# Optimization experiments

Hardware: AMD Instinct MI355X
Metric: run time of the kernel (lower is better)

The kernel has to match this reference:

```python
import jax, jax.numpy as jnp
import numpy as np

B, S, E, HD = 32, 1024, 768, 64
NUM_IMAGE_PATCHES = 49


def setup_inputs() -> dict:
    key = jax.random.key(0)
    ks = jax.random.split(key, 9)
    w = 0.02
    return {
        "decoder_sequence": jax.random.normal(ks[0], (B, S, E), dtype=jnp.float32),
        "Wq": jax.random.normal(ks[1], (E, HD), dtype=jnp.float32) * w,
        "bq": jnp.zeros((HD,), dtype=jnp.float32),
        "Wk": jax.random.normal(ks[2], (E, HD), dtype=jnp.float32) * w,
        "bk": jnp.zeros((HD,), dtype=jnp.float32),
        "Wv": jax.random.normal(ks[3], (E, HD), dtype=jnp.float32) * w,
        "bv": jnp.zeros((HD,), dtype=jnp.float32),
        "input_sequence_length": 975,
        "padding_mask": jax.random.randint(ks[4], (B, 1, S), 0, 2).astype(bool),
    }


def reference(decoder_sequence, Wq, bq, Wk, bk, Wv, bv, input_sequence_length, padding_mask):
    # single-head projections: [B,S,E] @ [E,HD] -> [B,S,HD]
    Q = decoder_sequence @ Wq + bq
    K = decoder_sequence @ Wk + bk
    V = decoder_sequence @ Wv + bv

    scores = jnp.einsum('bid,bjd->bij', Q, K) / jnp.sqrt(jnp.float32(HD))

    # mask: image-patch rows (i < 49) fully unmasked; text region is causal
    # (mask[49:,49:] = triu(-inf, diag=1)), i.e. -inf where i >= 49 and j > i.
    i = jnp.arange(S)[:, None]
    j = jnp.arange(S)[None, :]
    causal_bad = (i >= NUM_IMAGE_PATCHES) & (j > i)  # [S,S]
    scores = jnp.where(causal_bad[None, :, :], -jnp.inf, scores)

    # padding mask on keys, broadcast over queries: [B,1,S] -> [B,S,S]
    scores = jnp.where(padding_mask, -jnp.inf, scores)

    A = jax.nn.softmax(scores, axis=-1)
    H = jnp.einsum('bij,bjd->bid', A, V)
    return H
```

## Files before the change

kernel.cpp:

```cpp
#include <hip/hip_runtime.h>
#include <stdint.h>
#include <stddef.h>


typedef __attribute__((ext_vector_type(8))) short bf16x8;
typedef __attribute__((ext_vector_type(4))) float f32x4;

#define NIP 49
#define QSCALE 0.18033688011112042f

#define GLDS16(g, l)                                      \
  __builtin_amdgcn_global_load_lds(                       \
      (const __attribute__((address_space(1))) void*)(g), \
      (__attribute__((address_space(3))) void*)(l), 16, 0, 0)

__device__ __forceinline__ short f2b(float f) {
  union { float f; uint32_t u; } c; c.f = f;
  uint32_t u = c.u;
  uint32_t r = (u + 0x7fffu + ((u >> 16) & 1u)) >> 16;
  return (short)(uint16_t)r;
}

__device__ __forceinline__ uint32_t pk2(float lo, float hi) {
  uint32_t r;
  asm("v_cvt_pk_bf16_f32 %0, %1, %2" : "=v"(r) : "v"(lo), "v"(hi));
  return r;
}

__global__ __launch_bounds__(256) void wt_kernel(
    const float* __restrict__ Wq, const float* __restrict__ Wk,
    const float* __restrict__ Wv, const int* __restrict__ pad,
    short* __restrict__ Wt, float* __restrict__ padneg) {
  int idx = blockIdx.x * 256 + threadIdx.x;
  int m = idx / 49152;
  int idx2 = idx - m * 49152;
  int k = idx2 >> 6, n = idx2 & 63;
  const float* W = (m == 0) ? Wq : (m == 1) ? Wk : Wv;
  Wt[(size_t)(m * 64 + n) * 768 + k] = f2b(W[idx2]);
  if (idx < 32768) padneg[idx] = pad[idx] ? -16384.f : 0.f;
}

__global__ __launch_bounds__(256) void proj_kernel(
    const float* __restrict__ X, const float* __restrict__ bq,
    const float* __restrict__ bk, const float* __restrict__ bv,
    const short* __restrict__ Wt, short* __restrict__ Qg,
    short* __restrict__ Kg, short* __restrict__ Vt) {
  const int tid = threadIdx.x;
  const int wid = tid >> 6, lane = tid & 63;
  const int l15 = lane & 15, q4 = lane >> 4;
  const int r0 = blockIdx.x * 64;

  const float* xrow = X + (size_t)(r0 + wid * 16 + l15) * 768;
  float4 xa[2][4];
  auto xload = [&](int slot, int st) {
    const int kb = st * 64 + q4 * 8;
#pragma unroll
    for (int h = 0; h < 2; ++h) {
      xa[slot][h * 2 + 0] = *(const float4*)(xrow + kb + h * 32);
      xa[slot][h * 2 + 1] = *(const float4*)(xrow + kb + h * 32 + 4);
    }
  };
  auto mkfrag = [&](int slot, int h) {
    union { uint32_t u[4]; bf16x8 v; } r;
    const float4 a = xa[slot][h * 2], b = xa[slot][h * 2 + 1];
    r.u[0] = pk2(a.x, a.y); r.u[1] = pk2(a.z, a.w);
    r.u[2] = pk2(b.x, b.y); r.u[3] = pk2(b.z, b.w);
    return r.v;
  };

  const short* wrow = Wt + (size_t)l15 * 768 + q4 * 8;

  f32x4 acc[12];
#pragma unroll
  for (int c = 0; c < 12; ++c) acc[c] = (f32x4){0.f, 0.f, 0.f, 0.f};

  xload(0, 0);
  xload(1, 1);

#pragma unroll
  for (int st = 0; st < 12; ++st) {
    const int cur = st & 1;
    const bf16x8 a0 = mkfrag(cur, 0);
    const bf16x8 a1 = mkfrag(cur, 1);
    if (st + 2 < 12) xload(cur, st + 2);
#pragma unroll
    for (int c = 0; c < 12; ++c) {
      const short* wp = wrow + (size_t)c * 12288 + st * 64;
      const bf16x8 b0 = *(const bf16x8*)(wp);
      const bf16x8 b1 = *(const bf16x8*)(wp + 32);
      acc[c] = __builtin_amdgcn_mfma_f32_16x16x32_bf16(a0, b0, acc[c], 0, 0, 0);
      acc[c] = __builtin_amdgcn_mfma_f32_16x16x32_bf16(a1, b1, acc[c], 0, 0, 0);
    }
  }

  const int b = r0 >> 10, s0 = r0 & 1023;
#pragma unroll
  for (int c = 0; c < 12; ++c) {
    const int mtx = c >> 2;
    const int h = (c & 3) * 16 + l15;
    if (mtx < 2) {
      const float bias = (mtx == 0 ? bq : bk)[h];
      short* op = (mtx == 0) ? Qg : Kg;
#pragma unroll
      for (int rr = 0; rr < 4; ++rr) {
        int row = r0 + wid * 16 + q4 * 4 + rr;
        float v = acc[c][rr] + bias;
        if (mtx == 0) v *= QSCALE;
        op[(size_t)row * 64 + h] = f2b(v);
      }
    } else {
      const float bias = bv[h];
      uint2 sv;
      sv.x = pk2(acc[c][0] + bias, acc[c][1] + bias);
      sv.y = pk2(acc[c][2] + bias, acc[c][3] + bias);
      *(uint2*)(Vt + ((size_t)(b * 64 + h) << 10) + s0 + wid * 16 + q4 * 4) = sv;
    }
  }
}

__global__ __launch_bounds__(256, 2) void attn_kernel(
    const short* __restrict__ Qg, const short* __restrict__ Kg,
    const short* __restrict__ Vt, const float* __restrict__ padneg,
    float* __restrict__ out) {
  __shared__ short lK[2][2][128][32];
  __shared__ short lV[2][4][64][32];
  __shared__ short lOnes[16][32];

  const int b = blockIdx.x;
  const int level = blockIdx.y;
  const int t = (level == 0) ? 0 : 16 - level;
  const int tid = threadIdx.x;
  const int wid = tid >> 6, lane = tid & 63;
  const int l15 = lane & 15, q4 = lane >> 4;
  const int qs = t * 64;
  const size_t base = (size_t)b * 1024;
  const int nkt = (t == 0) ? 8 : (t / 2 + 1);

  {
    int i0 = tid, i1 = tid + 256;
    ((short*)lOnes)[i0] = ((i0 >> 5) == 0) ? (short)0x3F80 : (short)0;
    if (i1 < 512) ((short*)lOnes)[i1] = ((i1 >> 5) == 0) ? (short)0x3F80 : (short)0;
  }

  const short* qrow = Qg + (base + qs + wid * 16 + l15) * 64;
  bf16x8 bq0 = *(const bf16x8*)(qrow + q4 * 8);
  bf16x8 bq1 = *(const bf16x8*)(qrow + 32 + q4 * 8);
  const int qi = qs + wid * 16 + l15;

  const int sr = lane >> 2, sc = (lane & 3) * 8;
  auto wlds_tile = [&](int buf, int kt) {
    const int kb = kt * 128;
#pragma unroll
    for (int i = 0; i < 4; ++i) {
      const int dh = i & 1, krow = wid * 32 + (i >> 1) * 16;
      GLDS16(Kg + (base + kb + krow + sr) * 64 + dh * 32 + sc,
             &lK[buf][dh][krow][0]);
    }
#pragma unroll
    for (int kq = 0; kq < 4; ++kq) {
      GLDS16(Vt + ((size_t)(b * 64 + wid * 16 + sr) << 10) + kb + kq * 32 + sc,
             &lV[buf][kq][wid * 16][0]);
    }
  };

  float4 pnv[8];
  auto pnload = [&](int kt) {
#pragma unroll
    for (int c = 0; c < 8; ++c)
      pnv[c] = *(const float4*)(padneg + base + kt * 128 + c * 16 + q4 * 4);
  };

  pnload(0);
  wlds_tile(0, 0);
  __syncthreads();

  f32x4 o[5];
#pragma unroll
  for (int c = 0; c < 5; ++c) o[c] = (f32x4){0.f, 0.f, 0.f, 0.f};

  for (int kt = 0; kt < nkt; ++kt) {
    const int cur = kt & 1;
    const int kb = kt * 128;

    f32x4 s4[8];
#pragma unroll
    for (int c = 0; c < 8; ++c)
      s4[c] = (f32x4){pnv[c].x, pnv[c].y, pnv[c].z, pnv[c].w};

    if (kt + 1 < nkt) {
      wlds_tile(cur ^ 1, kt + 1);
      pnload(kt + 1);
    }

#pragma unroll
    for (int c = 0; c < 8; ++c) {
      bf16x8 a0 = *(const bf16x8*)&lK[cur][0][c * 16 + l15][q4 * 8];
      s4[c] = __builtin_amdgcn_mfma_f32_16x16x32_bf16(a0, bq0, s4[c], 0, 0, 0);
      bf16x8 a1 = *(const bf16x8*)&lK[cur][1][c * 16 + l15][q4 * 8];
      s4[c] = __builtin_amdgcn_mfma_f32_16x16x32_bf16(a1, bq1, s4[c], 0, 0, 0);
    }

    const bool diag = (t == 0) ? (kt == 0) : (kt == nkt - 1);
    const bool img = (t == 0 && kt > 0);
#pragma unroll
    for (int c = 0; c < 8; ++c) {
#pragma unroll
      for (int rr = 0; rr < 4; ++rr) {
        float pv = exp2f(fminf(s4[c][rr], 80.f));
        if (diag) {
          int j = kb + c * 16 + q4 * 4 + rr;
          if (qi >= NIP && j > qi) pv = 0.f;
        }
        if (img) {
          if (qi >= NIP) pv = 0.f;
        }
        s4[c][rr] = pv;
      }
    }

#pragma unroll
    for (int m = 0; m < 4; ++m) {
      uint32_t w0 = pk2(s4[2 * m][0], s4[2 * m][1]);
      uint32_t w1 = pk2(s4[2 * m][2], s4[2 * m][3]);
      uint32_t w2 = pk2(s4[2 * m + 1][0], s4[2 * m + 1][1]);
      uint32_t w3 = pk2(s4[2 * m + 1][2], s4[2 * m + 1][3]);
      asm("v_permlane32_swap_b32 %0, %1" : "+v"(w0), "+v"(w2));
      asm("v_permlane32_swap_b32 %0, %1" : "+v"(w1), "+v"(w3));
      asm("v_permlane16_swap_b32 %0, %1" : "+v"(w0), "+v"(w2));
      asm("v_permlane16_swap_b32 %0, %1" : "+v"(w1), "+v"(w3));
      union { uint32_t u[4]; bf16x8 v; } af;
      af.u[0] = w0; af.u[1] = w1; af.u[2] = w2; af.u[3] = w3;
#pragma unroll
      for (int c = 0; c < 5; ++c) {
        bf16x8 bv = (c < 4) ? *(const bf16x8*)&lV[cur][m][c * 16 + l15][q4 * 8]
                            : *(const bf16x8*)&lOnes[l15][q4 * 8];
        o[c] = __builtin_amdgcn_mfma_f32_16x16x32_bf16(af.v, bv, o[c], 0, 0, 0);
      }
    }
    __syncthreads();
  }

#pragma unroll
  for (int rr = 0; rr < 4; ++rr) {
    float l = __shfl(o[4][rr], lane & 48, 64);
    const float inv = (l > 0.f) ? 1.0f / l : 0.f;
    const size_t row = base + qs + wid * 16 + q4 * 4 + rr;
#pragma unroll
    for (int c = 0; c < 4; ++c)
      out[row * 64 + c * 16 + l15] = o[c][rr] * inv;
  }
}

extern "C" void kernel_launch(void* const* d_in, const int* in_sizes, int n_in,
                              void* d_out, int out_size, void* d_ws, size_t ws_size,
                              hipStream_t stream) {
  const float* X  = (const float*)d_in[0];
  const float* Wq = (const float*)d_in[1];
  const float* bq = (const float*)d_in[2];
  const float* Wk = (const float*)d_in[3];
  const float* bk = (const float*)d_in[4];
  const float* Wv = (const float*)d_in[5];
  const float* bv = (const float*)d_in[6];
  const int* pad  = (const int*)d_in[8];
  float* out = (float*)d_out;

  short* Qg = (short*)d_ws;
  short* Kg = Qg + 32768 * 64;
  short* Vt = Kg + 32768 * 64;
  short* Wt = Vt + 32768 * 64;
  float* padneg = (float*)(Wt + 147456);

  wt_kernel<<<576, 256, 0, stream>>>(Wq, Wk, Wv, pad, Wt, padneg);
  proj_kernel<<<512, 256, 0, stream>>>(X, bq, bk, bv, Wt, Qg, Kg, Vt);
  attn_kernel<<<dim3(32, 16), 256, 0, stream>>>(Qg, Kg, Vt, padneg, out);
}
```

Baseline: 243.5 us.

## Double per-wave row tile in projection and register-prefetch weight fragments

The projection kernel now has each wave compute two 16-row tiles instead of one, so every loaded weight fragment feeds two MFMAs. Weight fragments are prefetched into a double-buffered register array one k-step ahead, alongside the X loads. The grid is halved to 256 blocks with launch_bounds(256,1). The aim is to cut redundant global/L2 weight traffic and hide load latency, at the cost of much higher register pressure (48 accumulators plus 48 weight vectors) and fewer waves in flight.

```diff
diff --git a/kernel.cpp b/kernel.cpp
--- a/kernel.cpp
+++ b/kernel.cpp
@@ -31,16 +31,16 @@
     const float* __restrict__ Wq, const float* __restrict__ Wk,
     const float* __restrict__ Wv, const int* __restrict__ pad,
     short* __restrict__ Wt, float* __restrict__ padneg) {
-  int idx = blockIdx.x * 256 + threadIdx.x;
-  int m = idx / 49152;
-  int idx2 = idx - m * 49152;
+  int e = blockIdx.x * 256 + threadIdx.x;
+  int m = e / 49152;
+  int idx2 = e - m * 49152;
   int k = idx2 >> 6, n = idx2 & 63;
   const float* W = (m == 0) ? Wq : (m == 1) ? Wk : Wv;
   Wt[(size_t)(m * 64 + n) * 768 + k] = f2b(W[idx2]);
-  if (idx < 32768) padneg[idx] = pad[idx] ? -16384.f : 0.f;
-}
-
-__global__ __launch_bounds__(256) void proj_kernel(
+  if (e < 32768) padneg[e] = pad[e] ? -16384.f : 0.f;
+}
+
+__global__ __launch_bounds__(256, 1) void proj_kernel(
     const float* __restrict__ X, const float* __restrict__ bq,
     const float* __restrict__ bk, const float* __restrict__ bv,
     const short* __restrict__ Wt, short* __restrict__ Qg,
@@ -48,48 +48,68 @@
   const int tid = threadIdx.x;
   const int wid = tid >> 6, lane = tid & 63;
   const int l15 = lane & 15, q4 = lane >> 4;
-  const int r0 = blockIdx.x * 64;
-
-  const float* xrow = X + (size_t)(r0 + wid * 16 + l15) * 768;
-  float4 xa[2][4];
+  const int r0 = blockIdx.x * 128;
+  const int wr0 = r0 + wid * 32;
+
+  const float* xr0 = X + (size_t)(wr0 + l15) * 768;
+  const float* xr1 = xr0 + 16 * 768;
+  float4 xa[2][8];
   auto xload = [&](int slot, int st) {
     const int kb = st * 64 + q4 * 8;
 #pragma unroll
-    for (int h = 0; h < 2; ++h) {
-      xa[slot][h * 2 + 0] = *(const float4*)(xrow + kb + h * 32);
-      xa[slot][h * 2 + 1] = *(const float4*)(xrow + kb + h * 32 + 4);
-    }
-  };
-  auto mkfrag = [&](int slot, int h) {
+    for (int ks = 0; ks < 2; ++ks)
+#pragma unroll
+      for (int h = 0; h < 2; ++h) {
+        xa[slot][0 * 4 + ks * 2 + h] = *(const float4*)(xr0 + kb + ks * 32 + h * 4);
+        xa[slot][1 * 4 + ks * 2 + h] = *(const float4*)(xr1 + kb + ks * 32 + h * 4);
+      }
+  };
+  auto mkfrag = [&](int slot, int rt, int ks) {
     union { uint32_t u[4]; bf16x8 v; } r;
-    const float4 a = xa[slot][h * 2], b = xa[slot][h * 2 + 1];
+    const float4 a = xa[slot][rt * 4 + ks * 2 + 0];
+    const float4 b = xa[slot][rt * 4 + ks * 2 + 1];
     r.u[0] = pk2(a.x, a.y); r.u[1] = pk2(a.z, a.w);
     r.u[2] = pk2(b.x, b.y); r.u[3] = pk2(b.z, b.w);
     return r.v;
   };
 
-  const short* wrow = Wt + (size_t)l15 * 768 + q4 * 8;
-
-  f32x4 acc[12];
-#pragma unroll
-  for (int c = 0; c < 12; ++c) acc[c] = (f32x4){0.f, 0.f, 0.f, 0.f};
-
+  const short* wbase = Wt + (size_t)l15 * 768 + q4 * 8;
+  bf16x8 wv[2][24];
+  auto wload = [&](int slot, int st) {
+#pragma unroll
+    for (int ks = 0; ks < 2; ++ks)
+#pragma unroll
+      for (int c = 0; c < 12; ++c)
+        wv[slot][ks * 12 + c] =
+            *(const bf16x8*)(wbase + (size_t)c * 12288 + st * 64 + ks * 32);
+  };
+
+  f32x4 acc[2][12];
+#pragma unroll
+  for (int rt = 0; rt < 2; ++rt)
+#pragma unroll
+    for (int c = 0; c < 12; ++c) acc[rt][c] = (f32x4){0.f, 0.f, 0.f, 0.f};
+
+  wload(0, 0);
   xload(0, 0);
-  xload(1, 1);
 
 #pragma unroll
   for (int st = 0; st < 12; ++st) {
     const int cur = st & 1;
-    const bf16x8 a0 = mkfrag(cur, 0);
-    const bf16x8 a1 = mkfrag(cur, 1);
-    if (st + 2 < 12) xload(cur, st + 2);
-#pragma unroll
-    for (int c = 0; c < 12; ++c) {
-      const short* wp = wrow + (size_t)c * 12288 + st * 64;
-      const bf16x8 b0 = *(const bf16x8*)(wp);
-      const bf16x8 b1 = *(const bf16x8*)(wp + 32);
-      acc[c] = __builtin_amdgcn_mfma_f32_16x16x32_bf16(a0, b0, acc[c], 0, 0, 0);
-      acc[c] = __builtin_amdgcn_mfma_f32_16x16x32_bf16(a1, b1, acc[c], 0, 0, 0);
+    if (st + 1 < 12) {
+      wload(cur ^ 1, st + 1);
+      xload(cur ^ 1, st + 1);
+    }
+#pragma unroll
+    for (int ks = 0; ks < 2; ++ks) {
+      const bf16x8 a0 = mkfrag(cur, 0, ks);
+      const bf16x8 a1 = mkfrag(cur, 1, ks);
+#pragma unroll
+      for (int c = 0; c < 12; ++c) {
+        const bf16x8 bw = wv[cur][ks * 12 + c];
+        acc[0][c] = __builtin_amdgcn_mfma_f32_16x16x32_bf16(a0, bw, acc[0][c], 0, 0, 0);
+        acc[1][c] = __builtin_amdgcn_mfma_f32_16x16x32_bf16(a1, bw, acc[1][c], 0, 0, 0);
+      }
     }
   }
 
@@ -102,18 +122,24 @@
       const float bias = (mtx == 0 ? bq : bk)[h];
       short* op = (mtx == 0) ? Qg : Kg;
 #pragma unroll
-      for (int rr = 0; rr < 4; ++rr) {
-        int row = r0 + wid * 16 + q4 * 4 + rr;
-        float v = acc[c][rr] + bias;
-        if (mtx == 0) v *= QSCALE;
-        op[(size_t)row * 64 + h] = f2b(v);
-      }
+      for (int rt = 0; rt < 2; ++rt)
+#pragma unroll
+        for (int rr = 0; rr < 4; ++rr) {
+          int row = wr0 + rt * 16 + q4 * 4 + rr;
+          float v = acc[rt][c][rr] + bias;
+          if (mtx == 0) v *= QSCALE;
+          op[(size_t)row * 64 + h] = f2b(v);
+        }
     } else {
       const float bias = bv[h];
-      uint2 sv;
-      sv.x = pk2(acc[c][0] + bias, acc[c][1] + bias);
-      sv.y = pk2(acc[c][2] + bias, acc[c][3] + bias);
-      *(uint2*)(Vt + ((size_t)(b * 64 + h) << 10) + s0 + wid * 16 + q4 * 4) = sv;
+#pragma unroll
+      for (int rt = 0; rt < 2; ++rt) {
+        uint2 sv;
+        sv.x = pk2(acc[rt][c][0] + bias, acc[rt][c][1] + bias);
+        sv.y = pk2(acc[rt][c][2] + bias, acc[rt][c][3] + bias);
+        *(uint2*)(Vt + ((size_t)(b * 64 + h) << 10) +
+                  (s0 + wid * 32 + rt * 16 + q4 * 4)) = sv;
+      }
     }
   }
 }
@@ -271,6 +297,6 @@
   float* padneg = (float*)(Wt + 147456);
 
   wt_kernel<<<576, 256, 0, stream>>>(Wq, Wk, Wv, pad, Wt, padneg);
-  proj_kernel<<<512, 256, 0, stream>>>(X, bq, bk, bv, Wt, Qg, Kg, Vt);
+  proj_kernel<<<256, 256, 0, stream>>>(X, bq, bk, bv, Wt, Qg, Kg, Vt);
   attn_kernel<<<dim3(32, 16), 256, 0, stream>>>(Qg, Kg, Vt, padneg, out);
 }
```

Measured after the change: 240.2 us. Within noise of the previous version (-1.3%).
